# Performance work log

Hardware: AMD Instinct MI355X
Metric: run time of the kernel (lower is better)

Reference implementation:

```python
import jax, jax.numpy as jnp
import numpy as np
from jax import lax

U = 0.0  # fixed constant from __init__ (u=0.0), not trainable
PARAM_SCALE = 0.1  # keep the 2nd-order recurrence numerically stable over T=2048 steps


def setup_inputs() -> dict:
    key = jax.random.key(0)
    kx, kp, kt1, kt2, ke = jax.random.split(key, 5)
    B, T, H, W = 64, 2048, 16, 16
    return {
        "x": jax.random.normal(kx, (B, T, H, W), dtype=jnp.float32),
        "phi": jax.random.normal(kp, (1,), dtype=jnp.float32) * PARAM_SCALE,
        "theta_1": jax.random.normal(kt1, (1,), dtype=jnp.float32) * PARAM_SCALE,
        "theta_2": jax.random.normal(kt2, (1,), dtype=jnp.float32) * PARAM_SCALE,
        "e_0": jax.random.normal(ke, (1,), dtype=jnp.float32) * PARAM_SCALE,
    }


def reference(x, phi, theta_1, theta_2, e_0):
    # x: (B, T, H, W). Params are shape (1,), broadcast over (B, H, W) lanes.
    x0 = x[:, 0]  # (B, H, W)
    x1 = x[:, 1]
    y0 = x0 + U - theta_1 * e_0
    y1 = x1 + U + phi * (x1 - x0) - theta_1 * (x1 - y0) - theta_2 * e_0

    # time-major streams for t = 2 .. T-1
    x_t_seq = jnp.moveaxis(x[:, 2:], 1, 0)    # (T-2, B, H, W)
    x_tm1_seq = jnp.moveaxis(x[:, 1:-1], 1, 0)  # (T-2, B, H, W)

    def step(carry, inp):
        y_tm1, y_tm2 = carry
        x_t, x_tm1 = inp
        y_t = (x_t + U
               + phi * (x_t - x_tm1)
               - theta_1 * (x_t - y_tm1)
               - theta_2 * (x_tm1 - y_tm2))
        return (y_t, y_tm1), y_t

    _, ys = lax.scan(step, (y1, y0), (x_t_seq, x_tm1_seq))  # ys: (T-2, B, H, W)
    y = jnp.concatenate([y0[:, None], y1[:, None], jnp.moveaxis(ys, 0, 1)], axis=1)
    return y  # (B, T, H, W)
```

## Files before the change

kernel.cpp:

```cpp
#include <hip/hip_runtime.h>


#define T_DIM 2048
#define HW    256
#define HWV   64
#define CHUNK 128
#define WARM  64

__device__ __forceinline__ float4 arima_step(const float4 xt, const float4 xm1,
                                             const float4 ym1, const float4 ym2,
                                             const float ca, const float cb,
                                             const float t1, const float t2) {
    float4 r;
    r.x = fmaf(ca, xt.x, fmaf(cb, xm1.x, fmaf(t1, ym1.x, t2 * ym2.x)));
    r.y = fmaf(ca, xt.y, fmaf(cb, xm1.y, fmaf(t1, ym1.y, t2 * ym2.y)));
    r.z = fmaf(ca, xt.z, fmaf(cb, xm1.z, fmaf(t1, ym1.z, t2 * ym2.z)));
    r.w = fmaf(ca, xt.w, fmaf(cb, xm1.w, fmaf(t1, ym1.w, t2 * ym2.w)));
    return r;
}

__global__ __launch_bounds__(256) void arima_kernel(
    const float* __restrict__ x,
    const float* __restrict__ phi_p,
    const float* __restrict__ th1_p,
    const float* __restrict__ th2_p,
    const float* __restrict__ e0_p,
    float* __restrict__ y)
{
    const float phi = phi_p[0];
    const float t1  = th1_p[0];
    const float t2  = th2_p[0];
    const float e0  = e0_p[0];
    const float ca  = 1.0f + phi - t1;
    const float cb  = -(phi + t2);

    const int b     = blockIdx.x;
    const int chunk = blockIdx.y * blockDim.y + threadIdx.y;
    const int v     = threadIdx.x;

    const float4* __restrict__ xb =
        reinterpret_cast<const float4*>(x) + (size_t)b * T_DIM * HWV + v;
    float4* __restrict__ yb =
        reinterpret_cast<float4*>(y) + (size_t)b * T_DIM * HWV + v;

    float4 ym1, ym2, xm1;
    int t, tend;
    const int tstart = chunk * CHUNK;

    if (chunk == 0) {
        const float4 x0 = xb[0];
        const float4 x1 = xb[HWV];
        const float c0 = t1 * e0;
        const float c1 = t2 * e0;
        float4 y0, y1;
        y0.x = x0.x - c0; y0.y = x0.y - c0; y0.z = x0.z - c0; y0.w = x0.w - c0;
        y1.x = fmaf(ca, x1.x, fmaf(-phi, x0.x, fmaf(t1, y0.x, -c1)));
        y1.y = fmaf(ca, x1.y, fmaf(-phi, x0.y, fmaf(t1, y0.y, -c1)));
        y1.z = fmaf(ca, x1.z, fmaf(-phi, x0.z, fmaf(t1, y0.z, -c1)));
        y1.w = fmaf(ca, x1.w, fmaf(-phi, x0.w, fmaf(t1, y0.w, -c1)));
        yb[0]   = y0;
        yb[HWV] = y1;
        ym2 = y0; ym1 = y1; xm1 = x1;
        t = 2; tend = CHUNK;
    } else {
        const int ts = tstart - WARM;
        xm1 = xb[(size_t)(ts - 1) * HWV];
        ym1 = make_float4(0.f, 0.f, 0.f, 0.f);
        ym2 = ym1;
        #pragma unroll 4
        for (t = ts; t < tstart; ++t) {
            const float4 xt = xb[(size_t)t * HWV];
            const float4 yt = arima_step(xt, xm1, ym1, ym2, ca, cb, t1, t2);
            ym2 = ym1; ym1 = yt; xm1 = xt;
        }
        tend = tstart + CHUNK;
    }

    #pragma unroll 4
    for (; t < tend; ++t) {
        const float4 xt = xb[(size_t)t * HWV];
        const float4 yt = arima_step(xt, xm1, ym1, ym2, ca, cb, t1, t2);
        yb[(size_t)t * HWV] = yt;
        ym2 = ym1; ym1 = yt; xm1 = xt;
    }
}

extern "C" void kernel_launch(void* const* d_in, const int* in_sizes, int n_in,
                              void* d_out, int out_size, void* d_ws, size_t ws_size,
                              hipStream_t stream) {
    const float* x    = (const float*)d_in[0];
    const float* phi  = (const float*)d_in[1];
    const float* th1  = (const float*)d_in[2];
    const float* th2  = (const float*)d_in[3];
    const float* e0   = (const float*)d_in[4];
    float* y          = (float*)d_out;

    const int B = in_sizes[0] / (T_DIM * HW);
    const int nchunk = T_DIM / CHUNK;
    dim3 block(HWV, 4);
    dim3 grid(B, nchunk / 4);
    arima_kernel<<<grid, block, 0, stream>>>(x, phi, th1, th2, e0, y);
}
```

Before: 255.0 us.

## Use scalar per-lane recurrence with one chunk per block

Each thread now handles one scalar (h,w) lane instead of a float4, so a 256-thread block covers all 256 lanes of a single time chunk. The grid becomes chunks by batch rather than grouping four chunks per block. Unroll factors rise from 4 to 8. The goal is four times as many independent threads in flight, giving more parallelism to hide load latency in the serial recurrence. In exchange, memory accesses become 4-byte per lane instead of 16-byte vector loads, which means more load/store instructions.

```diff
diff --git a/kernel.cpp b/kernel.cpp
--- a/kernel.cpp
+++ b/kernel.cpp
@@ -3,21 +3,8 @@
 
 #define T_DIM 2048
 #define HW    256
-#define HWV   64
 #define CHUNK 128
 #define WARM  64
-
-__device__ __forceinline__ float4 arima_step(const float4 xt, const float4 xm1,
-                                             const float4 ym1, const float4 ym2,
-                                             const float ca, const float cb,
-                                             const float t1, const float t2) {
-    float4 r;
-    r.x = fmaf(ca, xt.x, fmaf(cb, xm1.x, fmaf(t1, ym1.x, t2 * ym2.x)));
-    r.y = fmaf(ca, xt.y, fmaf(cb, xm1.y, fmaf(t1, ym1.y, t2 * ym2.y)));
-    r.z = fmaf(ca, xt.z, fmaf(cb, xm1.z, fmaf(t1, ym1.z, t2 * ym2.z)));
-    r.w = fmaf(ca, xt.w, fmaf(cb, xm1.w, fmaf(t1, ym1.w, t2 * ym2.w)));
-    return r;
-}
 
 __global__ __launch_bounds__(256) void arima_kernel(
     const float* __restrict__ x,
@@ -34,53 +21,44 @@
     const float ca  = 1.0f + phi - t1;
     const float cb  = -(phi + t2);
 
-    const int b     = blockIdx.x;
-    const int chunk = blockIdx.y * blockDim.y + threadIdx.y;
-    const int v     = threadIdx.x;
+    const int chunk = blockIdx.x;
+    const int b     = blockIdx.y;
+    const int hw    = threadIdx.x;
 
-    const float4* __restrict__ xb =
-        reinterpret_cast<const float4*>(x) + (size_t)b * T_DIM * HWV + v;
-    float4* __restrict__ yb =
-        reinterpret_cast<float4*>(y) + (size_t)b * T_DIM * HWV + v;
+    const float* __restrict__ xb = x + (size_t)b * T_DIM * HW + hw;
+    float* __restrict__ yb       = y + (size_t)b * T_DIM * HW + hw;
 
-    float4 ym1, ym2, xm1;
+    float ym1, ym2, xm1;
     int t, tend;
     const int tstart = chunk * CHUNK;
 
     if (chunk == 0) {
-        const float4 x0 = xb[0];
-        const float4 x1 = xb[HWV];
-        const float c0 = t1 * e0;
-        const float c1 = t2 * e0;
-        float4 y0, y1;
-        y0.x = x0.x - c0; y0.y = x0.y - c0; y0.z = x0.z - c0; y0.w = x0.w - c0;
-        y1.x = fmaf(ca, x1.x, fmaf(-phi, x0.x, fmaf(t1, y0.x, -c1)));
-        y1.y = fmaf(ca, x1.y, fmaf(-phi, x0.y, fmaf(t1, y0.y, -c1)));
-        y1.z = fmaf(ca, x1.z, fmaf(-phi, x0.z, fmaf(t1, y0.z, -c1)));
-        y1.w = fmaf(ca, x1.w, fmaf(-phi, x0.w, fmaf(t1, y0.w, -c1)));
-        yb[0]   = y0;
-        yb[HWV] = y1;
+        const float x0 = xb[0];
+        const float x1 = xb[HW];
+        const float y0 = x0 - t1 * e0;
+        const float y1 = fmaf(ca, x1, fmaf(-phi, x0, fmaf(t1, y0, -(t2 * e0))));
+        yb[0]  = y0;
+        yb[HW] = y1;
         ym2 = y0; ym1 = y1; xm1 = x1;
         t = 2; tend = CHUNK;
     } else {
         const int ts = tstart - WARM;
-        xm1 = xb[(size_t)(ts - 1) * HWV];
-        ym1 = make_float4(0.f, 0.f, 0.f, 0.f);
-        ym2 = ym1;
-        #pragma unroll 4
+        xm1 = xb[(size_t)(ts - 1) * HW];
+        ym1 = 0.0f; ym2 = 0.0f;
+        #pragma unroll 8
         for (t = ts; t < tstart; ++t) {
-            const float4 xt = xb[(size_t)t * HWV];
-            const float4 yt = arima_step(xt, xm1, ym1, ym2, ca, cb, t1, t2);
+            const float xt = xb[(size_t)t * HW];
+            const float yt = fmaf(ca, xt, fmaf(cb, xm1, fmaf(t1, ym1, t2 * ym2)));
             ym2 = ym1; ym1 = yt; xm1 = xt;
         }
         tend = tstart + CHUNK;
     }
 
-    #pragma unroll 4
+    #pragma unroll 8
     for (; t < tend; ++t) {
-        const float4 xt = xb[(size_t)t * HWV];
-        const float4 yt = arima_step(xt, xm1, ym1, ym2, ca, cb, t1, t2);
-        yb[(size_t)t * HWV] = yt;
+        const float xt = xb[(size_t)t * HW];
+        const float yt = fmaf(ca, xt, fmaf(cb, xm1, fmaf(t1, ym1, t2 * ym2)));
+        yb[(size_t)t * HW] = yt;
         ym2 = ym1; ym1 = yt; xm1 = xt;
     }
 }
@@ -97,7 +75,7 @@
 
     const int B = in_sizes[0] / (T_DIM * HW);
     const int nchunk = T_DIM / CHUNK;
-    dim3 block(HWV, 4);
-    dim3 grid(B, nchunk / 4);
+    dim3 block(HW);
+    dim3 grid(nchunk, B);
     arima_kernel<<<grid, block, 0, stream>>>(x, phi, th1, th2, e0, y);
 }
```

Measured after the change: 253.6 us. Within noise of the previous version (-0.6%).
